# Performance work log

Measured on AMD Instinct MI355X. Metric: run time of the kernel, lower is better.

The kernel has to match this reference:

```python
import jax, jax.numpy as jnp
import numpy as np


def conv2d(x, w, b):
    pad = (w.shape[-1] - 1) // 2
    y = jax.lax.conv_general_dilated(x, w, (1, 1), [(pad, pad), (pad, pad)],
                                     dimension_numbers=('NCHW', 'OIHW', 'NCHW'))
    return y + b[None, :, None, None]


def mish(x):
    return x * jnp.tanh(jax.nn.softplus(x))


def setup_inputs() -> dict:
    key = jax.random.key(0)
    ks = jax.random.split(key, 8)
    B, C, H, W = 8, 16, 256, 256
    s = 0.1
    return dict(
        x=jax.random.normal(ks[0], (B, C, H, W), jnp.float32),
        W1=jax.random.normal(ks[1], (4, 1, 3, 3), jnp.float32) * s,      # conv1: 1->4, k=3
        b1=jnp.zeros((4,), jnp.float32),
        Wred=jax.random.normal(ks[2], (1, 4, 1, 1), jnp.float32) * s,    # involution reduce 4->1
        bred=jnp.zeros((1,), jnp.float32),
        Wspan=jax.random.normal(ks[3], (9, 1, 1, 1), jnp.float32) * s,   # involution span 1->k^2
        bspan=jnp.zeros((9,), jnp.float32),
        W2=jax.random.normal(ks[4], (C, 4 * C, 3, 3), jnp.float32) * s,  # conv2: 4C->C, k=3
        b2=jnp.zeros((C,), jnp.float32),
        Weca=jax.random.normal(ks[5], (3,), jnp.float32) * s,            # ECA 1D conv kernel
    )


def reference(x, W1, b1, Wred, bred, Wspan, bspan, W2, b2, Weca):
    B, C, H, W = x.shape
    H2 = H // 2
    K2 = 9  # 3x3 involution kernel
    # per-channel 1->4 conv + Mish: vectorize the Python channel loop by folding C into batch
    xs = x.reshape(B * C, 1, H, W)
    f = mish(conv2d(xs, W1, b1))                      # (B*C, 4, H, W)
    top, bot = f[:, :, :H2], f[:, :, H2:]             # each (B*C, 4, H2, W)
    # involution2(y1, y2): dynamic per-pixel 3x3 kernel from bottom half, applied to top half
    ker = conv2d(jax.nn.relu(conv2d(bot, Wred, bred)), Wspan, bspan)   # (B*C, 9, H2, W)
    patches = jax.lax.conv_general_dilated_patches(
        top, (3, 3), (1, 1), [(1, 1), (1, 1)],
        dimension_numbers=('NCHW', 'OIHW', 'NCHW'))                    # (B*C, 4*9, H2, W), channel-major
    patches = patches.reshape(B * C, 4, K2, H2, W)
    top_inv = (patches * ker[:, None]).sum(axis=2)                     # (B*C, 4, H2, W)
    # shuffle/concat: out channel-block i = [inv_top_i ; bottom_{(i+1) % C}] along height
    ti = top_inv.reshape(B, C, 4, H2, W)
    bo = bot.reshape(B, C, 4, H2, W)
    shuffled = jnp.concatenate([ti, jnp.roll(bo, -1, axis=1)], axis=3)  # (B, C, 4, H, W)
    shuffled = shuffled.reshape(B, 4 * C, H, W)
    out = mish(conv2d(shuffled, W2, b2))               # (B, C, H, W)
    # ECA: gate from global-avg-pooled `out`, 1D cross-correlation (k=3, pad=1) over channels
    pooled = out.mean(axis=(2, 3))                     # (B, C)
    yp = jnp.pad(pooled, ((0, 0), (1, 1)))
    gate = jax.nn.sigmoid(Weca[0] * yp[:, :-2] + Weca[1] * yp[:, 1:-1] + Weca[2] * yp[:, 2:])
    return x * gate[:, :, None, None]
```

## Files before the change

### kernel.cpp

```cpp
#include <hip/hip_runtime.h>
#include <hip/hip_bf16.h>

#define H 256
#define Wd 256
#define H2 128

typedef unsigned short ushort_t;
typedef __attribute__((ext_vector_type(8))) short short8;
typedef __attribute__((ext_vector_type(4))) float f32x4;

__device__ __forceinline__ float mishf(float v){
  if (v > 15.f) return v;
  float e = __expf(v);
  float w = e*(e+2.f);
  return v * w * __builtin_amdgcn_rcpf(w + 2.f);
}

__device__ __forceinline__ ushort_t f2bf(float f){
  unsigned int u = __float_as_uint(f);
  u += 0x7fffu + ((u >> 16) & 1u);
  return (ushort_t)(u >> 16);
}
__device__ __forceinline__ float bf2f(ushort_t h){
  return __uint_as_float(((unsigned int)h) << 16);
}


__global__ void k0_pack(const float* __restrict__ W2, ushort_t* __restrict__ wpack)
{
  int idx = blockIdx.x*128 + threadIdx.x;
  if (idx >= 1152) return;
  int lane  = idx & 63;
  int s     = (idx >> 6) % 9;
  int khalf = idx / 576;
  int n = lane & 15, g = lane >> 4;
  unsigned int w[4];
#pragma unroll
  for (int h = 0; h < 4; ++h){
    int ch0 = khalf*32 + g*8 + 2*h;
    unsigned lo = f2bf(W2[(n*64 + ch0  )*9 + s]);
    unsigned hi = f2bf(W2[(n*64 + ch0+1)*9 + s]);
    w[h] = lo | (hi << 16);
  }
  *(uint4*)(wpack + (size_t)idx*8) = make_uint4(w[0], w[1], w[2], w[3]);
}

__global__ __launch_bounds__(256) void k1_bot(
    const float* __restrict__ x, const float* __restrict__ W1,
    const float* __restrict__ b1, ushort_t* __restrict__ shuf)
{
  int bid = blockIdx.x;
  int n   = bid >> 5;
  int rg  = bid & 31;
  int tid = threadIdx.x;
  int i   = 128 + rg*4 + (tid >> 6);
  int j0  = (tid & 63) * 4;
  const float* xp = x + (size_t)n * (H*Wd);

  float w[4][9], bb[4];
#pragma unroll
  for (int m=0;m<4;m++){
    bb[m] = b1[m];
#pragma unroll
    for (int k=0;k<9;k++) w[m][k] = W1[m*9+k];
  }

  float xv[3][6];
#pragma unroll
  for (int r=0;r<3;r++){
    int row = i-1+r;
    bool rok = (row < H);
#pragma unroll
    for (int c=0;c<6;c++){
      int col = j0-1+c;
      xv[r][c] = (rok && col>=0 && col<Wd) ? xp[row*Wd+col] : 0.f;
    }
  }

  int b = n >> 4, cs = n & 15;
  int cdst = (cs + 15) & 15;
  float o[4][4];
#pragma unroll
  for (int m=0;m<4;m++){
#pragma unroll
    for (int p=0;p<4;p++){
      float s = bb[m];
#pragma unroll
      for (int ky=0;ky<3;ky++)
#pragma unroll
        for (int kx=0;kx<3;kx++)
          s = fmaf(xv[ky][p+kx], w[m][ky*3+kx], s);
      o[m][p] = mishf(s);
    }
  }
  size_t pbase = ((size_t)(b*16 + cdst))*65536 + (size_t)i*256 + j0;
#pragma unroll
  for (int p=0;p<4;p++){
    ushort4 hv;
    hv.x = f2bf(o[0][p]); hv.y = f2bf(o[1][p]);
    hv.z = f2bf(o[2][p]); hv.w = f2bf(o[3][p]);
    *(ushort4*)(shuf + (pbase + p)*4) = hv;
  }
}

__global__ __launch_bounds__(256) void k2_top(
    const float* __restrict__ x, const float* __restrict__ W1,
    const float* __restrict__ b1, const float* __restrict__ Wred,
    const float* __restrict__ bred, const float* __restrict__ Wspan,
    const float* __restrict__ bspan, ushort_t* __restrict__ shuf)
{
  __shared__ float xt[20][69];
  __shared__ float ft[4][18][69];

  int bid = blockIdx.x;
  int n   = bid >> 5;
  int t   = bid & 31;
  int itop0 = (t >> 2) * 16;
  int j0    = (t & 3) * 64;
  int tid = threadIdx.x;
  const float* xp = x + (size_t)n * (H*Wd);

  float w1r[4][9], b1r[4], wredr[4], wsp[9], bsp[9];
  float bredr = bred[0];
#pragma unroll
  for (int m=0;m<4;m++){
    b1r[m] = b1[m]; wredr[m] = Wred[m];
#pragma unroll
    for (int k=0;k<9;k++) w1r[m][k] = W1[m*9+k];
  }
#pragma unroll
  for (int k=0;k<9;k++){ wsp[k] = Wspan[k]; bsp[k] = bspan[k]; }

  for (int idx=tid; idx<20*68; idx+=256){
    int r = idx/68, c = idx - r*68;
    int row = itop0-2+r, col = j0-2+c;
    xt[r][c] = (row>=0 && col>=0 && col<Wd) ? xp[row*Wd+col] : 0.f;
  }
  __syncthreads();

  for (int idx=tid; idx<18*66; idx+=256){
    int r = idx/66, c = idx - r*66;
    int frow = itop0-1+r, fcol = j0-1+c;
    bool ok = (frow>=0 && frow<H2 && fcol<Wd && fcol>=0);
    float xv[3][3];
#pragma unroll
    for (int ky=0;ky<3;ky++)
#pragma unroll
      for (int kx=0;kx<3;kx++) xv[ky][kx] = xt[r+ky][c+kx];
#pragma unroll
    for (int m=0;m<4;m++){
      float s = b1r[m];
#pragma unroll
      for (int ky=0;ky<3;ky++)
#pragma unroll
        for (int kx=0;kx<3;kx++)
          s = fmaf(xv[ky][kx], w1r[m][ky*3+kx], s);
      ft[m][r][c] = ok ? mishf(s) : 0.f;
    }
  }
  __syncthreads();

  int lr  = tid >> 4;
  int lc4 = (tid & 15) * 4;
  int trow = itop0 + lr;
  int bq = n >> 4, cq = n & 15;

  int nb = bq*16 + ((cq + 15) & 15);
  const ushort4* fbp = (const ushort4*)(shuf +
      ((size_t)nb*65536 + (size_t)(128+trow)*256 + (j0+lc4))*4);
  float gv[4];
#pragma unroll
  for (int p=0;p<4;p++){
    ushort4 rec = fbp[p];
    float s = bredr;
    s = fmaf(bf2f(rec.x), wredr[0], s);
    s = fmaf(bf2f(rec.y), wredr[1], s);
    s = fmaf(bf2f(rec.z), wredr[2], s);
    s = fmaf(bf2f(rec.w), wredr[3], s);
    gv[p] = fmaxf(s, 0.f);
  }

  float o[4][4];
#pragma unroll
  for (int m=0;m<4;m++){
    float fv[3][6];
#pragma unroll
    for (int ky=0;ky<3;ky++)
#pragma unroll
      for (int c=0;c<6;c++)
        fv[ky][c] = ft[m][lr+ky][lc4+c];
#pragma unroll
    for (int p=0;p<4;p++){
      float A = 0.f, Bv = 0.f;
#pragma unroll
      for (int ky=0;ky<3;ky++)
#pragma unroll
        for (int kx=0;kx<3;kx++){
          A  = fmaf(fv[ky][p+kx], wsp[ky*3+kx], A);
          Bv = fmaf(fv[ky][p+kx], bsp[ky*3+kx], Bv);
        }
      o[m][p] = fmaf(gv[p], A, Bv);
    }
  }
  size_t pbase = ((size_t)(bq*16 + cq))*65536 + (size_t)trow*256 + j0 + lc4;
#pragma unroll
  for (int p=0;p<4;p++){
    ushort4 hv;
    hv.x = f2bf(o[0][p]); hv.y = f2bf(o[1][p]);
    hv.z = f2bf(o[2][p]); hv.w = f2bf(o[3][p]);
    *(ushort4*)(shuf + (pbase + p)*4) = hv;
  }
}

__global__ __launch_bounds__(256) void k3_conv2(
    const ushort_t* __restrict__ shuf, const ushort_t* __restrict__ wpack,
    const float* __restrict__ b2, float* __restrict__ scratch)
{
  __shared__ f32x4 mg[2][8][64];
  __shared__ float pacc[16];

  int bid0 = blockIdx.x;
  int bid  = (bid0 & 7)*256 + (bid0 >> 3);
  int b   = bid >> 8;
  int t   = bid & 255;
  int rb  = t >> 3;
  int cb  = t & 7;
  int tid = threadIdx.x;
  int lane = tid & 63;
  int n = lane & 15;
  int g = lane >> 4;
  int wid = tid >> 6;
  int colhalf = wid & 1;
  int khalf   = wid >> 1;

  if (tid < 16) pacc[tid] = 0.f;

  const short8* wp = (const short8*)wpack + (size_t)khalf*576 + lane;
  short8 afr[9];
#pragma unroll
  for (int s = 0; s < 9; ++s) afr[s] = wp[s*64];

  f32x4 acc[8];
#pragma unroll
  for (int r = 0; r < 8; ++r) acc[r] = f32x4{0.f,0.f,0.f,0.f};

  int r0 = rb*8 - 1;
  int c  = cb*32 - 1 + colhalf*16 + n;
  int p0 = khalf*8 + g*2;
  const ushort_t* sp = shuf + ((size_t)(b*16 + p0))*262144;

#pragma unroll
  for (int hr = 0; hr < 10; ++hr){
    int grow = r0 + hr;
    bool rok = (unsigned)grow < 256u;
    uint2 va[3], vb[3];
#pragma unroll
    for (int kx = 0; kx < 3; ++kx){
      int gcol = c + kx;
      uint2 a = make_uint2(0u,0u), bv = make_uint2(0u,0u);
      if (rok && (unsigned)gcol < 256u){
        const ushort_t* pp = sp + (size_t)(grow*256 + gcol)*4;
        a  = *(const uint2*)pp;
        bv = *(const uint2*)(pp + 262144);
      }
      va[kx] = a; vb[kx] = bv;
    }
#pragma unroll
    for (int kx = 0; kx < 3; ++kx){
      union { uint4 u; short8 s; } cv;
      cv.u = make_uint4(va[kx].x, va[kx].y, vb[kx].x, vb[kx].y);
#pragma unroll
      for (int ky = 0; ky < 3; ++ky){
        int orow = hr - ky;
        if (orow >= 0 && orow < 8){
          acc[orow] = __builtin_amdgcn_mfma_f32_16x16x32_bf16(
              afr[ky*3+kx], cv.s, acc[orow], 0, 0, 0);
        }
      }
    }
  }

  if (khalf == 1){
#pragma unroll
    for (int r = 0; r < 8; ++r) mg[colhalf][r][lane] = acc[r];
  }
  __syncthreads();

  if (khalf == 0){
    float b2v[4];
#pragma unroll
    for (int q = 0; q < 4; ++q) b2v[q] = b2[g*4 + q];
    float po[4] = {0.f, 0.f, 0.f, 0.f};
#pragma unroll
    for (int r = 0; r < 8; ++r){
      f32x4 o = acc[r] + mg[colhalf][r][lane];
#pragma unroll
      for (int q = 0; q < 4; ++q) po[q] += mishf(o[q] + b2v[q]);
    }
#pragma unroll
    for (int q = 0; q < 4; ++q){
#pragma unroll
      for (int mk = 1; mk < 16; mk <<= 1) po[q] += __shfl_xor(po[q], mk);
    }
    if (n == 0){
#pragma unroll
      for (int q = 0; q < 4; ++q) atomicAdd(&pacc[g*4 + q], po[q]);
    }
  }
  __syncthreads();
  if (tid < 16) scratch[bid*16 + tid] = pacc[tid];
}

__global__ void k4_gate(const float* __restrict__ scratch,
                        const float* __restrict__ Weca,
                        float* __restrict__ gate)
{
  __shared__ float rr[16][16];
  __shared__ float pool[16];
  int b = blockIdx.x;
  int t = threadIdx.x;
  int oc = t & 15, ch = t >> 4;
  float s = 0.f;
  for (int u = 0; u < 16; ++u)
    s += scratch[(size_t)(b*256 + ch*16 + u)*16 + oc];
  rr[ch][oc] = s;
  __syncthreads();
  if (t < 16){
    float tot = 0.f;
#pragma unroll
    for (int k = 0; k < 16; ++k) tot += rr[k][t];
    pool[t] = tot * (1.0f/65536.0f);
  }
  __syncthreads();
  if (t < 16){
    float pm = (t > 0)  ? pool[t-1] : 0.f;
    float p0 = pool[t];
    float pp = (t < 15) ? pool[t+1] : 0.f;
    float z = Weca[0]*pm + Weca[1]*p0 + Weca[2]*pp;
    gate[b*16 + t] = 1.f/(1.f + __expf(-z));
  }
}

__global__ __launch_bounds__(256) void k5_scale(
    const float4* __restrict__ x4, const float* __restrict__ gate,
    float4* __restrict__ out4)
{
  int idx = blockIdx.x*256 + threadIdx.x;
  float g = gate[idx >> 14];
  float4 v = x4[idx];
  v.x *= g; v.y *= g; v.z *= g; v.w *= g;
  out4[idx] = v;
}

extern "C" void kernel_launch(void* const* d_in, const int* in_sizes, int n_in,
                              void* d_out, int out_size, void* d_ws, size_t ws_size,
                              hipStream_t stream)
{
  const float* x     = (const float*)d_in[0];
  const float* W1    = (const float*)d_in[1];
  const float* b1    = (const float*)d_in[2];
  const float* Wred  = (const float*)d_in[3];
  const float* bred  = (const float*)d_in[4];
  const float* Wspan = (const float*)d_in[5];
  const float* bspan = (const float*)d_in[6];
  const float* W2    = (const float*)d_in[7];
  const float* b2    = (const float*)d_in[8];
  const float* Weca  = (const float*)d_in[9];

  ushort_t* shuf    = (ushort_t*)d_ws;
  float*    gate    = (float*)((char*)d_ws + 67108864);
  ushort_t* wpack   = (ushort_t*)((char*)d_ws + 67108864 + 1024);
  float*    scratch = (float*)d_out;

  k0_pack<<<9, 128, 0, stream>>>(W2, wpack);
  k1_bot <<<4096, 256, 0, stream>>>(x, W1, b1, shuf);
  k2_top <<<4096, 256, 0, stream>>>(x, W1, b1, Wred, bred, Wspan, bspan, shuf);
  k3_conv2<<<2048, 256, 0, stream>>>(shuf, wpack, b2, scratch);
  k4_gate<<<8, 256, 0, stream>>>(scratch, Weca, gate);
  k5_scale<<<8192, 256, 0, stream>>>((const float4*)x, gate, (float4*)d_out);
}
```

Before: 99.25 us.

## Fuse bottom-half conv into involution kernel, use packed FMA and nontemporal stores

Merges the separate bottom-half conv1+Mish kernel into the top-half involution kernel. Each block now loads the matching bottom rows of x into shared memory, computes the bottom features in registers, writes them to the shuffle buffer, and uses the fp32 values directly for the involution kernel generation. This removes one launch and the write-then-reread of bf16 bottom features, and the span weights now use full-precision inputs instead of bf16-rounded ones. Inner loops are also packed into 2-wide float vectors to get packed FMA, and the final scale kernel uses nontemporal stores. The costs are more shared memory and registers per block, which may lower occupancy.

```diff
diff --git a/kernel.cpp b/kernel.cpp
--- a/kernel.cpp
+++ b/kernel.cpp
@@ -8,6 +8,7 @@
 typedef unsigned short ushort_t;
 typedef __attribute__((ext_vector_type(8))) short short8;
 typedef __attribute__((ext_vector_type(4))) float f32x4;
+typedef __attribute__((ext_vector_type(2))) float f32x2;
 
 __device__ __forceinline__ float mishf(float v){
   if (v > 15.f) return v;
@@ -45,71 +46,14 @@
   *(uint4*)(wpack + (size_t)idx*8) = make_uint4(w[0], w[1], w[2], w[3]);
 }
 
-__global__ __launch_bounds__(256) void k1_bot(
-    const float* __restrict__ x, const float* __restrict__ W1,
-    const float* __restrict__ b1, ushort_t* __restrict__ shuf)
-{
-  int bid = blockIdx.x;
-  int n   = bid >> 5;
-  int rg  = bid & 31;
-  int tid = threadIdx.x;
-  int i   = 128 + rg*4 + (tid >> 6);
-  int j0  = (tid & 63) * 4;
-  const float* xp = x + (size_t)n * (H*Wd);
-
-  float w[4][9], bb[4];
-#pragma unroll
-  for (int m=0;m<4;m++){
-    bb[m] = b1[m];
-#pragma unroll
-    for (int k=0;k<9;k++) w[m][k] = W1[m*9+k];
-  }
-
-  float xv[3][6];
-#pragma unroll
-  for (int r=0;r<3;r++){
-    int row = i-1+r;
-    bool rok = (row < H);
-#pragma unroll
-    for (int c=0;c<6;c++){
-      int col = j0-1+c;
-      xv[r][c] = (rok && col>=0 && col<Wd) ? xp[row*Wd+col] : 0.f;
-    }
-  }
-
-  int b = n >> 4, cs = n & 15;
-  int cdst = (cs + 15) & 15;
-  float o[4][4];
-#pragma unroll
-  for (int m=0;m<4;m++){
-#pragma unroll
-    for (int p=0;p<4;p++){
-      float s = bb[m];
-#pragma unroll
-      for (int ky=0;ky<3;ky++)
-#pragma unroll
-        for (int kx=0;kx<3;kx++)
-          s = fmaf(xv[ky][p+kx], w[m][ky*3+kx], s);
-      o[m][p] = mishf(s);
-    }
-  }
-  size_t pbase = ((size_t)(b*16 + cdst))*65536 + (size_t)i*256 + j0;
-#pragma unroll
-  for (int p=0;p<4;p++){
-    ushort4 hv;
-    hv.x = f2bf(o[0][p]); hv.y = f2bf(o[1][p]);
-    hv.z = f2bf(o[2][p]); hv.w = f2bf(o[3][p]);
-    *(ushort4*)(shuf + (pbase + p)*4) = hv;
-  }
-}
-
-__global__ __launch_bounds__(256) void k2_top(
+__global__ __launch_bounds__(256) void k12(
     const float* __restrict__ x, const float* __restrict__ W1,
     const float* __restrict__ b1, const float* __restrict__ Wred,
     const float* __restrict__ bred, const float* __restrict__ Wspan,
     const float* __restrict__ bspan, ushort_t* __restrict__ shuf)
 {
   __shared__ float xt[20][69];
+  __shared__ float xb[18][69];
   __shared__ float ft[4][18][69];
 
   int bid = blockIdx.x;
@@ -120,65 +64,100 @@
   int tid = threadIdx.x;
   const float* xp = x + (size_t)n * (H*Wd);
 
-  float w1r[4][9], b1r[4], wredr[4], wsp[9], bsp[9];
+  f32x2 w01[9], w23[9], b01, b23, wspb[9];
+  float wredr[4];
   float bredr = bred[0];
 #pragma unroll
-  for (int m=0;m<4;m++){
-    b1r[m] = b1[m]; wredr[m] = Wred[m];
-#pragma unroll
-    for (int k=0;k<9;k++) w1r[m][k] = W1[m*9+k];
-  }
-#pragma unroll
-  for (int k=0;k<9;k++){ wsp[k] = Wspan[k]; bsp[k] = bspan[k]; }
+  for (int k=0;k<9;k++){
+    w01[k] = f32x2{W1[k], W1[9+k]};
+    w23[k] = f32x2{W1[18+k], W1[27+k]};
+    wspb[k] = f32x2{Wspan[k], bspan[k]};
+  }
+  b01 = f32x2{b1[0], b1[1]};
+  b23 = f32x2{b1[2], b1[3]};
+#pragma unroll
+  for (int m=0;m<4;m++) wredr[m] = Wred[m];
 
   for (int idx=tid; idx<20*68; idx+=256){
     int r = idx/68, c = idx - r*68;
     int row = itop0-2+r, col = j0-2+c;
     xt[r][c] = (row>=0 && col>=0 && col<Wd) ? xp[row*Wd+col] : 0.f;
   }
+  for (int idx=tid; idx<18*68; idx+=256){
+    int r = idx/68, c = idx - r*68;
+    int row = 127+itop0+r, col = j0-2+c;
+    xb[r][c] = (row<H && col>=0 && col<Wd) ? xp[row*Wd+col] : 0.f;
+  }
   __syncthreads();
 
   for (int idx=tid; idx<18*66; idx+=256){
     int r = idx/66, c = idx - r*66;
     int frow = itop0-1+r, fcol = j0-1+c;
-    bool ok = (frow>=0 && frow<H2 && fcol<Wd && fcol>=0);
-    float xv[3][3];
+    bool ok = (frow>=0 && frow<H2 && fcol>=0 && fcol<Wd);
+    f32x2 s01 = b01, s23 = b23;
 #pragma unroll
     for (int ky=0;ky<3;ky++)
 #pragma unroll
-      for (int kx=0;kx<3;kx++) xv[ky][kx] = xt[r+ky][c+kx];
-#pragma unroll
-    for (int m=0;m<4;m++){
-      float s = b1r[m];
-#pragma unroll
-      for (int ky=0;ky<3;ky++)
-#pragma unroll
-        for (int kx=0;kx<3;kx++)
-          s = fmaf(xv[ky][kx], w1r[m][ky*3+kx], s);
-      ft[m][r][c] = ok ? mishf(s) : 0.f;
-    }
-  }
-  __syncthreads();
+      for (int kx=0;kx<3;kx++){
+        float xv = xt[r+ky][c+kx];
+        f32x2 xv2 = f32x2{xv, xv};
+        s01 = xv2*w01[ky*3+kx] + s01;
+        s23 = xv2*w23[ky*3+kx] + s23;
+      }
+    ft[0][r][c] = ok ? mishf(s01.x) : 0.f;
+    ft[1][r][c] = ok ? mishf(s01.y) : 0.f;
+    ft[2][r][c] = ok ? mishf(s23.x) : 0.f;
+    ft[3][r][c] = ok ? mishf(s23.y) : 0.f;
+  }
 
   int lr  = tid >> 4;
   int lc4 = (tid & 15) * 4;
   int trow = itop0 + lr;
   int bq = n >> 4, cq = n & 15;
 
-  int nb = bq*16 + ((cq + 15) & 15);
-  const ushort4* fbp = (const ushort4*)(shuf +
-      ((size_t)nb*65536 + (size_t)(128+trow)*256 + (j0+lc4))*4);
+  float fb[4][4];
+  {
+    float xv[3][6];
+#pragma unroll
+    for (int r=0;r<3;r++)
+#pragma unroll
+      for (int c=0;c<6;c++)
+        xv[r][c] = xb[lr+r][lc4+1+c];
+#pragma unroll
+    for (int p=0;p<4;p++){
+      f32x2 s01 = b01, s23 = b23;
+#pragma unroll
+      for (int ky=0;ky<3;ky++)
+#pragma unroll
+        for (int kx=0;kx<3;kx++){
+          float v = xv[ky][p+kx];
+          f32x2 v2 = f32x2{v, v};
+          s01 = v2*w01[ky*3+kx] + s01;
+          s23 = v2*w23[ky*3+kx] + s23;
+        }
+      fb[0][p] = mishf(s01.x); fb[1][p] = mishf(s01.y);
+      fb[2][p] = mishf(s23.x); fb[3][p] = mishf(s23.y);
+    }
+  }
+  int cdst = (cq + 15) & 15;
+  size_t bbase = ((size_t)(bq*16 + cdst))*65536 + (size_t)(128+trow)*256 + j0 + lc4;
+#pragma unroll
+  for (int p=0;p<4;p++){
+    ushort4 hv;
+    hv.x = f2bf(fb[0][p]); hv.y = f2bf(fb[1][p]);
+    hv.z = f2bf(fb[2][p]); hv.w = f2bf(fb[3][p]);
+    *(ushort4*)(shuf + (bbase + p)*4) = hv;
+  }
   float gv[4];
 #pragma unroll
   for (int p=0;p<4;p++){
-    ushort4 rec = fbp[p];
     float s = bredr;
-    s = fmaf(bf2f(rec.x), wredr[0], s);
-    s = fmaf(bf2f(rec.y), wredr[1], s);
-    s = fmaf(bf2f(rec.z), wredr[2], s);
-    s = fmaf(bf2f(rec.w), wredr[3], s);
+#pragma unroll
+    for (int m=0;m<4;m++) s = fmaf(fb[m][p], wredr[m], s);
     gv[p] = fmaxf(s, 0.f);
   }
+
+  __syncthreads();
 
   float o[4][4];
 #pragma unroll
@@ -191,15 +170,15 @@
         fv[ky][c] = ft[m][lr+ky][lc4+c];
 #pragma unroll
     for (int p=0;p<4;p++){
-      float A = 0.f, Bv = 0.f;
+      f32x2 ab = f32x2{0.f, 0.f};
 #pragma unroll
       for (int ky=0;ky<3;ky++)
 #pragma unroll
         for (int kx=0;kx<3;kx++){
-          A  = fmaf(fv[ky][p+kx], wsp[ky*3+kx], A);
-          Bv = fmaf(fv[ky][p+kx], bsp[ky*3+kx], Bv);
+          float fvv = fv[ky][p+kx];
+          ab = f32x2{fvv, fvv}*wspb[ky*3+kx] + ab;
         }
-      o[m][p] = fmaf(gv[p], A, Bv);
+      o[m][p] = fmaf(gv[p], ab.x, ab.y);
     }
   }
   size_t pbase = ((size_t)(bq*16 + cq))*65536 + (size_t)trow*256 + j0 + lc4;
@@ -342,14 +321,13 @@
 }
 
 __global__ __launch_bounds__(256) void k5_scale(
-    const float4* __restrict__ x4, const float* __restrict__ gate,
-    float4* __restrict__ out4)
+    const f32x4* __restrict__ x4, const float* __restrict__ gate,
+    f32x4* __restrict__ out4)
 {
   int idx = blockIdx.x*256 + threadIdx.x;
   float g = gate[idx >> 14];
-  float4 v = x4[idx];
-  v.x *= g; v.y *= g; v.z *= g; v.w *= g;
-  out4[idx] = v;
+  f32x4 v = x4[idx] * g;
+  __builtin_nontemporal_store(v, &out4[idx]);
 }
 
 extern "C" void kernel_launch(void* const* d_in, const int* in_sizes, int n_in,
@@ -373,9 +351,8 @@
   float*    scratch = (float*)d_out;
 
   k0_pack<<<9, 128, 0, stream>>>(W2, wpack);
-  k1_bot <<<4096, 256, 0, stream>>>(x, W1, b1, shuf);
-  k2_top <<<4096, 256, 0, stream>>>(x, W1, b1, Wred, bred, Wspan, bspan, shuf);
+  k12    <<<4096, 256, 0, stream>>>(x, W1, b1, Wred, bred, Wspan, bspan, shuf);
   k3_conv2<<<2048, 256, 0, stream>>>(shuf, wpack, b2, scratch);
   k4_gate<<<8, 256, 0, stream>>>(scratch, Weca, gate);
-  k5_scale<<<8192, 256, 0, stream>>>((const float4*)x, gate, (float4*)d_out);
-}
+  k5_scale<<<8192, 256, 0, stream>>>((const f32x4*)x, gate, (f32x4*)d_out);
+}
```

Result: faster. 90.61 us (-8.7%).
